# Kernel tuning notes

Measured on AMD Instinct MI355X. Metric: run time of the kernel, lower is better.

The kernel has to match this reference:

```python
import jax, jax.numpy as jnp
import numpy as np


def setup_inputs() -> dict:
    key = jax.random.key(0)
    ks = jax.random.split(key, 5)
    B, T, D, H = 64, 1024, 512, 1024
    s = 1.0 / np.sqrt(H)
    return {
        "x": jax.random.normal(ks[0], (B, T, D), dtype=jnp.float32),
        "W_ih": jax.random.normal(ks[1], (3 * H, D), dtype=jnp.float32) * s,
        "W_hh": jax.random.normal(ks[2], (3 * H, H), dtype=jnp.float32) * s,
        "b_ih": jax.random.normal(ks[3], (3 * H,), dtype=jnp.float32) * s,
        "b_hh": jax.random.normal(ks[4], (3 * H,), dtype=jnp.float32) * s,
    }


def reference(x, W_ih, W_hh, b_ih, b_hh):
    # GRULayer: per-timestep GRU cell recurrence, zero initial hidden state.
    B, T, D = x.shape
    H = W_hh.shape[1]
    h0 = jnp.zeros((B, H), dtype=x.dtype)
    xT = jnp.swapaxes(x, 0, 1)  # [T, B, D]

    def step(h, x_t):
        gi = x_t @ W_ih.T + b_ih          # [B, 3H]
        gh = h @ W_hh.T + b_hh            # [B, 3H]
        i_r, i_z, i_n = jnp.split(gi, 3, axis=-1)
        h_r, h_z, h_n = jnp.split(gh, 3, axis=-1)
        r = jax.nn.sigmoid(i_r + h_r)
        z = jax.nn.sigmoid(i_z + h_z)
        n = jnp.tanh(i_n + r * h_n)
        h_new = (1.0 - z) * n + z * h
        return h_new, h_new

    h_final, outs = jax.lax.scan(step, h0, xT)  # outs: [T, B, H]
    res = jnp.swapaxes(outs, 0, 1)              # [B, T, H]
    return res, h_final
```

## Files before the change

kernel.cpp:

```cpp
#include <hip/hip_runtime.h>
#include <hip/hip_bf16.h>

#define NB 64
#define TT 1024
#define ND 512
#define NH 1024
#define GRID 256
#define NTH 256

typedef float f32x4 __attribute__((ext_vector_type(4)));
typedef __bf16 bf16x8 __attribute__((ext_vector_type(8)));

__device__ __forceinline__ float sigmoid_f(float v) { return 1.0f / (1.0f + __expf(-v)); }

__device__ __forceinline__ float tanh_f(float v) {
    float a = fabsf(v);
    float e = __expf(-2.0f * a);
    float t = (1.0f - e) / (1.0f + e);
    return copysignf(t, v);
}

__device__ __forceinline__ f32x4 load_dwordx4_sc1(const void* p) {
    f32x4 r;
    asm volatile("global_load_dwordx4 %0, %1, off sc1" : "=v"(r) : "v"(p));
    return r;
}
__device__ __forceinline__ void store_short_sc1(void* p, unsigned v16) {
    asm volatile("global_store_short %0, %1, off sc1" :: "v"(p), "v"(v16) : "memory");
}
__device__ __forceinline__ void store_dword_sc1(unsigned* p, unsigned v) {
    asm volatile("global_store_dword %0, %1, off sc1" :: "v"(p), "v"(v) : "memory");
}
__device__ __forceinline__ unsigned load_dword_sc1_wait(const unsigned* p) {
    unsigned v;
    asm volatile("global_load_dword %0, %1, off sc1\n\ts_waitcnt vmcnt(0)"
                 : "=v"(v) : "v"(p) : "memory");
    return v;
}

__global__ void __launch_bounds__(NTH) gru_kernel(
    const float* __restrict__ x, const float* __restrict__ W_ih,
    const float* __restrict__ W_hh, const float* __restrict__ b_ih,
    const float* __restrict__ b_hh, float* __restrict__ out,
    unsigned* __restrict__ tags, __bf16* __restrict__ hbuf)
{
    extern __shared__ char smem[];
    __bf16* WihF = (__bf16*)smem;
    __bf16* WhhF = WihF + 4 * 4 * 3 * 64 * 8;
    float* prz = (float*)(WhhF + 4 * 8 * 3 * 64 * 8);
    float* pnx = prz + 2048;
    float* pnh = pnx + 1024;

    const int tid = threadIdx.x;
    const int bg = blockIdx.x >> 6;
    const int cg = blockIdx.x & 63;
    const int brow = bg << 4;
    const int hc0 = cg << 4;

    for (int s = tid; s < 4 * 4 * 3 * 64; s += NTH) {
        int ln = s & 63, r = s >> 6;
        int g = r % 3, r2 = r / 3;
        int it = r2 & 3, w = r2 >> 2;
        int k = w * 128 + it * 32 + (ln >> 4) * 8;
        int col = ln & 15;
        const float* src = W_ih + (size_t)(g * NH + hc0 + col) * ND + k;
        float4 va = *(const float4*)(src);
        float4 vb = *(const float4*)(src + 4);
        bf16x8 f;
        f[0] = (__bf16)va.x; f[1] = (__bf16)va.y; f[2] = (__bf16)va.z; f[3] = (__bf16)va.w;
        f[4] = (__bf16)vb.x; f[5] = (__bf16)vb.y; f[6] = (__bf16)vb.z; f[7] = (__bf16)vb.w;
        *(bf16x8*)(WihF + (size_t)s * 8) = f;
    }
    for (int s = tid; s < 4 * 8 * 3 * 64; s += NTH) {
        int ln = s & 63, r = s >> 6;
        int g = r % 3, r2 = r / 3;
        int it = r2 & 7, w = r2 >> 3;
        int k = w * 256 + it * 32 + (ln >> 4) * 8;
        int col = ln & 15;
        const float* src = W_hh + (size_t)(g * NH + hc0 + col) * NH + k;
        float4 va = *(const float4*)(src);
        float4 vb = *(const float4*)(src + 4);
        bf16x8 f;
        f[0] = (__bf16)va.x; f[1] = (__bf16)va.y; f[2] = (__bf16)va.z; f[3] = (__bf16)va.w;
        f[4] = (__bf16)vb.x; f[5] = (__bf16)vb.y; f[6] = (__bf16)vb.z; f[7] = (__bf16)vb.w;
        *(bf16x8*)(WhhF + (size_t)s * 8) = f;
    }

    const int jcol = tid & 15;
    const int mrow = tid >> 4;
    const float b_r = b_ih[hc0 + jcol] + b_hh[hc0 + jcol];
    const float b_z = b_ih[NH + hc0 + jcol] + b_hh[NH + hc0 + jcol];
    const float b_nx = b_ih[2 * NH + hc0 + jcol];
    const float b_nh = b_hh[2 * NH + hc0 + jcol];

    __syncthreads();

    const int wave = tid >> 6;
    const int lane = tid & 63;
    const int lrow = lane & 15;
    const int kgrp = lane >> 4;

    unsigned* mytag = tags + ((size_t)(bg * 64 + cg) * 16 + wave);
    const unsigned* polltag = tags + ((size_t)(bg * 64 + wave * 16 + (lane >> 2)) * 16 + (lane & 3));

    __bf16* hst0 = hbuf + (size_t)NB * NH + (size_t)(brow + mrow) * NH + hc0 + jcol;
    __bf16* hst1 = hbuf + (size_t)(brow + mrow) * NH + hc0 + jcol;

    float hp = 0.0f;

    f32x4 xa[4], xb[4];
    {
        const float* xr = x + ((size_t)(brow + lrow) * TT + 0) * ND + wave * 128 + kgrp * 8;
        #pragma unroll
        for (int it = 0; it < 4; ++it) {
            xa[it] = *(const f32x4*)(xr + it * 32);
            xb[it] = *(const f32x4*)(xr + it * 32 + 4);
        }
    }

    for (int t = 0; t < TT; ++t) {
        const int par = t & 1;
        f32x4 ar{}, az{}, anx{}, anh{};

        #pragma unroll
        for (int it = 0; it < 4; ++it) {
            bf16x8 af;
            af[0] = (__bf16)xa[it][0]; af[1] = (__bf16)xa[it][1];
            af[2] = (__bf16)xa[it][2]; af[3] = (__bf16)xa[it][3];
            af[4] = (__bf16)xb[it][0]; af[5] = (__bf16)xb[it][1];
            af[6] = (__bf16)xb[it][2]; af[7] = (__bf16)xb[it][3];
            const __bf16* wp = WihF + ((size_t)(wave * 4 + it) * 3) * 512 + lane * 8;
            bf16x8 wr = *(const bf16x8*)(wp);
            bf16x8 wz = *(const bf16x8*)(wp + 512);
            bf16x8 wn = *(const bf16x8*)(wp + 1024);
            ar  = __builtin_amdgcn_mfma_f32_16x16x32_bf16(af, wr, ar, 0, 0, 0);
            az  = __builtin_amdgcn_mfma_f32_16x16x32_bf16(af, wz, az, 0, 0, 0);
            anx = __builtin_amdgcn_mfma_f32_16x16x32_bf16(af, wn, anx, 0, 0, 0);
        }

        if (t > 0) {
            const unsigned tgt = (unsigned)t;
            for (;;) {
                unsigned v = load_dword_sc1_wait(polltag);
                if (__all(v == tgt)) break;
                __builtin_amdgcn_s_sleep(1);
            }
        }

        const __bf16* hrow = hbuf + (size_t)par * NB * NH + (size_t)(brow + lrow) * NH
                           + wave * 256 + kgrp * 8;
        f32x4 hraw[8];
        #pragma unroll
        for (int it = 0; it < 8; ++it)
            hraw[it] = load_dwordx4_sc1(hrow + it * 32);
        asm volatile("s_waitcnt vmcnt(0)" ::: "memory");
        __builtin_amdgcn_sched_barrier(0);
        #pragma unroll
        for (int it = 0; it < 8; ++it) {
            bf16x8 af = __builtin_bit_cast(bf16x8, hraw[it]);
            const __bf16* wp = WhhF + ((size_t)(wave * 8 + it) * 3) * 512 + lane * 8;
            bf16x8 wr = *(const bf16x8*)(wp);
            bf16x8 wz = *(const bf16x8*)(wp + 512);
            bf16x8 wn = *(const bf16x8*)(wp + 1024);
            ar  = __builtin_amdgcn_mfma_f32_16x16x32_bf16(af, wr, ar, 0, 0, 0);
            az  = __builtin_amdgcn_mfma_f32_16x16x32_bf16(af, wz, az, 0, 0, 0);
            anh = __builtin_amdgcn_mfma_f32_16x16x32_bf16(af, wn, anh, 0, 0, 0);
        }

        if (t + 1 < TT) {
            const float* xn = x + ((size_t)(brow + lrow) * TT + (t + 1)) * ND
                            + wave * 128 + kgrp * 8;
            #pragma unroll
            for (int it = 0; it < 4; ++it) {
                xa[it] = *(const f32x4*)(xn + it * 32);
                xb[it] = *(const f32x4*)(xn + it * 32 + 4);
            }
        }

        #pragma unroll
        for (int j = 0; j < 4; ++j) {
            int row = kgrp * 4 + j;
            prz[wave * 512 + row * 32 + lrow]      = ar[j];
            prz[wave * 512 + row * 32 + 16 + lrow] = az[j];
            pnx[wave * 256 + row * 16 + lrow]      = anx[j];
            pnh[wave * 256 + row * 16 + lrow]      = anh[j];
        }
        __syncthreads();

        {
            float rpre = prz[mrow * 32 + jcol] + prz[512 + mrow * 32 + jcol]
                       + prz[1024 + mrow * 32 + jcol] + prz[1536 + mrow * 32 + jcol] + b_r;
            float zpre = prz[mrow * 32 + 16 + jcol] + prz[512 + mrow * 32 + 16 + jcol]
                       + prz[1024 + mrow * 32 + 16 + jcol] + prz[1536 + mrow * 32 + 16 + jcol] + b_z;
            float ginn = pnx[mrow * 16 + jcol] + pnx[256 + mrow * 16 + jcol]
                       + pnx[512 + mrow * 16 + jcol] + pnx[768 + mrow * 16 + jcol] + b_nx;
            float ghnn = pnh[mrow * 16 + jcol] + pnh[256 + mrow * 16 + jcol]
                       + pnh[512 + mrow * 16 + jcol] + pnh[768 + mrow * 16 + jcol] + b_nh;
            float r = sigmoid_f(rpre);
            float z = sigmoid_f(zpre);
            float n = tanh_f(ginn + r * ghnn);
            float hn = (1.0f - z) * n + z * hp;
            hp = hn;

            unsigned hb = (unsigned)__builtin_bit_cast(unsigned short, (__bf16)hn);
            store_short_sc1(par ? hst1 : hst0, hb);
            asm volatile("s_waitcnt vmcnt(0)" ::: "memory");
            if (t < TT - 1 && lane == 0)
                store_dword_sc1(mytag, (unsigned)(t + 1));

            out[((size_t)(brow + mrow) * TT + t) * NH + hc0 + jcol] = hn;
            if (t == TT - 1)
                out[(size_t)NB * TT * NH + (size_t)(brow + mrow) * NH + hc0 + jcol] = hn;
        }

        __syncthreads();
    }
}

extern "C" void kernel_launch(void* const* d_in, const int* in_sizes, int n_in,
                              void* d_out, int out_size, void* d_ws, size_t ws_size,
                              hipStream_t stream) {
    (void)in_sizes; (void)n_in; (void)out_size;
    const float* x    = (const float*)d_in[0];
    const float* W_ih = (const float*)d_in[1];
    const float* W_hh = (const float*)d_in[2];
    const float* b_ih = (const float*)d_in[3];
    const float* b_hh = (const float*)d_in[4];
    float* out = (float*)d_out;

    unsigned* tags = (unsigned*)d_ws;
    __bf16* hbuf = (__bf16*)((char*)d_ws + 16384);
    const size_t clear_bytes = 16384 + (size_t)NB * NH * sizeof(__bf16);
    if (ws_size < 16384 + (size_t)2 * NB * NH * sizeof(__bf16)) return;
    hipMemsetAsync(d_ws, 0, clear_bytes, stream);

    const size_t smem_bytes = 163840;
    (void)hipFuncSetAttribute((const void*)gru_kernel,
                              hipFuncAttributeMaxDynamicSharedMemorySize, (int)smem_bytes);
    gru_kernel<<<GRID, NTH, smem_bytes, stream>>>(x, W_ih, W_hh, b_ih, b_hh, out, tags, hbuf);
}
```

Baseline: 3.751 ms.

## Embed step tags into hidden-state words to remove separate flag handshake

Each hidden value is now stored as a 32-bit word that carries the bf16 value in the low half and the timestep tag in the high half. Consumers read the data directly and check every tag, so the separate tag store, the wait on store completion, and the flag polling are gone. Readers fall back to polling a single word when the tags do not match. The next-step x prefetch is also moved before the wait. The cost is twice the hidden-buffer traffic and extra repacking ALU work, and correctness now depends on each 32-bit store being seen atomically.

```diff
diff --git a/kernel.cpp b/kernel.cpp
--- a/kernel.cpp
+++ b/kernel.cpp
@@ -9,6 +9,7 @@
 #define NTH 256
 
 typedef float f32x4 __attribute__((ext_vector_type(4)));
+typedef unsigned u32x4 __attribute__((ext_vector_type(4)));
 typedef __bf16 bf16x8 __attribute__((ext_vector_type(8)));
 
 __device__ __forceinline__ float sigmoid_f(float v) { return 1.0f / (1.0f + __expf(-v)); }
@@ -20,13 +21,11 @@
     return copysignf(t, v);
 }
 
-__device__ __forceinline__ f32x4 load_dwordx4_sc1(const void* p) {
-    f32x4 r;
-    asm volatile("global_load_dwordx4 %0, %1, off sc1" : "=v"(r) : "v"(p));
+__device__ __forceinline__ u32x4 load_dwordx4_sc1_off(const unsigned* p, int imm) {
+    u32x4 r;
+    asm volatile("global_load_dwordx4 %0, %1, off offset:%2 sc1"
+                 : "=v"(r) : "v"(p), "i"(imm));
     return r;
-}
-__device__ __forceinline__ void store_short_sc1(void* p, unsigned v16) {
-    asm volatile("global_store_short %0, %1, off sc1" :: "v"(p), "v"(v16) : "memory");
 }
 __device__ __forceinline__ void store_dword_sc1(unsigned* p, unsigned v) {
     asm volatile("global_store_dword %0, %1, off sc1" :: "v"(p), "v"(v) : "memory");
@@ -42,7 +41,7 @@
     const float* __restrict__ x, const float* __restrict__ W_ih,
     const float* __restrict__ W_hh, const float* __restrict__ b_ih,
     const float* __restrict__ b_hh, float* __restrict__ out,
-    unsigned* __restrict__ tags, __bf16* __restrict__ hbuf)
+    unsigned* __restrict__ hbuf)
 {
     extern __shared__ char smem[];
     __bf16* WihF = (__bf16*)smem;
@@ -100,11 +99,9 @@
     const int lrow = lane & 15;
     const int kgrp = lane >> 4;
 
-    unsigned* mytag = tags + ((size_t)(bg * 64 + cg) * 16 + wave);
-    const unsigned* polltag = tags + ((size_t)(bg * 64 + wave * 16 + (lane >> 2)) * 16 + (lane & 3));
-
-    __bf16* hst0 = hbuf + (size_t)NB * NH + (size_t)(brow + mrow) * NH + hc0 + jcol;
-    __bf16* hst1 = hbuf + (size_t)(brow + mrow) * NH + hc0 + jcol;
+    const size_t hoff_c = (size_t)(brow + lrow) * NH + wave * 256 + kgrp * 8;
+    const size_t hoff_cn = (size_t)(brow + 4 * (lane & 3)) * NH + wave * 256 + (lane >> 2) * 16;
+    const size_t hoff_p = (size_t)(brow + mrow) * NH + hc0 + jcol;
 
     float hp = 0.0f;
 
@@ -138,26 +135,57 @@
             anx = __builtin_amdgcn_mfma_f32_16x16x32_bf16(af, wn, anx, 0, 0, 0);
         }
 
-        if (t > 0) {
-            const unsigned tgt = (unsigned)t;
+        if (t + 1 < TT) {
+            const float* xn = x + ((size_t)(brow + lrow) * TT + (t + 1)) * ND
+                            + wave * 128 + kgrp * 8;
+            #pragma unroll
+            for (int it = 0; it < 4; ++it) {
+                xa[it] = *(const f32x4*)(xn + it * 32);
+                xb[it] = *(const f32x4*)(xn + it * 32 + 4);
+            }
+        }
+
+        const unsigned tag = (unsigned)t;
+        const unsigned* hbase = hbuf + (size_t)par * NB * NH + hoff_c;
+        const unsigned* cbase = hbuf + (size_t)par * NB * NH + hoff_cn;
+        u32x4 hw[16];
+        for (;;) {
+            hw[0]  = load_dwordx4_sc1_off(hbase,   0); hw[1]  = load_dwordx4_sc1_off(hbase,  16);
+            hw[2]  = load_dwordx4_sc1_off(hbase, 128); hw[3]  = load_dwordx4_sc1_off(hbase, 144);
+            hw[4]  = load_dwordx4_sc1_off(hbase, 256); hw[5]  = load_dwordx4_sc1_off(hbase, 272);
+            hw[6]  = load_dwordx4_sc1_off(hbase, 384); hw[7]  = load_dwordx4_sc1_off(hbase, 400);
+            hw[8]  = load_dwordx4_sc1_off(hbase, 512); hw[9]  = load_dwordx4_sc1_off(hbase, 528);
+            hw[10] = load_dwordx4_sc1_off(hbase, 640); hw[11] = load_dwordx4_sc1_off(hbase, 656);
+            hw[12] = load_dwordx4_sc1_off(hbase, 768); hw[13] = load_dwordx4_sc1_off(hbase, 784);
+            hw[14] = load_dwordx4_sc1_off(hbase, 896); hw[15] = load_dwordx4_sc1_off(hbase, 912);
+            asm volatile("s_waitcnt vmcnt(0)" ::: "memory");
+            __builtin_amdgcn_sched_barrier(0);
+            unsigned acc = 0;
+            #pragma unroll
+            for (int i = 0; i < 16; ++i) {
+                acc |= ((hw[i][0] >> 16) ^ tag);
+                acc |= ((hw[i][1] >> 16) ^ tag);
+                acc |= ((hw[i][2] >> 16) ^ tag);
+                acc |= ((hw[i][3] >> 16) ^ tag);
+            }
+            if (__all(acc == 0)) break;
             for (;;) {
-                unsigned v = load_dword_sc1_wait(polltag);
-                if (__all(v == tgt)) break;
+                unsigned c = load_dword_sc1_wait(cbase);
+                if (__all((c >> 16) == tag)) break;
                 __builtin_amdgcn_s_sleep(1);
             }
         }
-
-        const __bf16* hrow = hbuf + (size_t)par * NB * NH + (size_t)(brow + lrow) * NH
-                           + wave * 256 + kgrp * 8;
-        f32x4 hraw[8];
-        #pragma unroll
-        for (int it = 0; it < 8; ++it)
-            hraw[it] = load_dwordx4_sc1(hrow + it * 32);
-        asm volatile("s_waitcnt vmcnt(0)" ::: "memory");
         __builtin_amdgcn_sched_barrier(0);
+
         #pragma unroll
         for (int it = 0; it < 8; ++it) {
-            bf16x8 af = __builtin_bit_cast(bf16x8, hraw[it]);
+            u32x4 a = hw[2 * it], b = hw[2 * it + 1];
+            u32x4 d;
+            d[0] = (a[0] & 0xffffu) | (a[1] << 16);
+            d[1] = (a[2] & 0xffffu) | (a[3] << 16);
+            d[2] = (b[0] & 0xffffu) | (b[1] << 16);
+            d[3] = (b[2] & 0xffffu) | (b[3] << 16);
+            bf16x8 af = __builtin_bit_cast(bf16x8, d);
             const __bf16* wp = WhhF + ((size_t)(wave * 8 + it) * 3) * 512 + lane * 8;
             bf16x8 wr = *(const bf16x8*)(wp);
             bf16x8 wz = *(const bf16x8*)(wp + 512);
@@ -165,16 +193,6 @@
             ar  = __builtin_amdgcn_mfma_f32_16x16x32_bf16(af, wr, ar, 0, 0, 0);
             az  = __builtin_amdgcn_mfma_f32_16x16x32_bf16(af, wz, az, 0, 0, 0);
             anh = __builtin_amdgcn_mfma_f32_16x16x32_bf16(af, wn, anh, 0, 0, 0);
-        }
-
-        if (t + 1 < TT) {
-            const float* xn = x + ((size_t)(brow + lrow) * TT + (t + 1)) * ND
-                            + wave * 128 + kgrp * 8;
-            #pragma unroll
-            for (int it = 0; it < 4; ++it) {
-                xa[it] = *(const f32x4*)(xn + it * 32);
-                xb[it] = *(const f32x4*)(xn + it * 32 + 4);
-            }
         }
 
         #pragma unroll
@@ -202,12 +220,11 @@
             float hn = (1.0f - z) * n + z * hp;
             hp = hn;
 
-            unsigned hb = (unsigned)__builtin_bit_cast(unsigned short, (__bf16)hn);
-            store_short_sc1(par ? hst1 : hst0, hb);
-            asm volatile("s_waitcnt vmcnt(0)" ::: "memory");
-            if (t < TT - 1 && lane == 0)
-                store_dword_sc1(mytag, (unsigned)(t + 1));
-
+            if (t < TT - 1) {
+                unsigned hb = (unsigned)__builtin_bit_cast(unsigned short, (__bf16)hn);
+                unsigned hword = ((unsigned)(t + 1) << 16) | hb;
+                store_dword_sc1(hbuf + (size_t)((t + 1) & 1) * NB * NH + hoff_p, hword);
+            }
             out[((size_t)(brow + mrow) * TT + t) * NH + hc0 + jcol] = hn;
             if (t == TT - 1)
                 out[(size_t)NB * TT * NH + (size_t)(brow + mrow) * NH + hc0 + jcol] = hn;
@@ -228,14 +245,13 @@
     const float* b_hh = (const float*)d_in[4];
     float* out = (float*)d_out;
 
-    unsigned* tags = (unsigned*)d_ws;
-    __bf16* hbuf = (__bf16*)((char*)d_ws + 16384);
-    const size_t clear_bytes = 16384 + (size_t)NB * NH * sizeof(__bf16);
-    if (ws_size < 16384 + (size_t)2 * NB * NH * sizeof(__bf16)) return;
-    hipMemsetAsync(d_ws, 0, clear_bytes, stream);
+    unsigned* hbuf = (unsigned*)d_ws;
+    const size_t need = (size_t)2 * NB * NH * sizeof(unsigned);
+    if (ws_size < need) return;
+    hipMemsetAsync(d_ws, 0, need, stream);
 
     const size_t smem_bytes = 163840;
     (void)hipFuncSetAttribute((const void*)gru_kernel,
                               hipFuncAttributeMaxDynamicSharedMemorySize, (int)smem_bytes);
-    gru_kernel<<<GRID, NTH, smem_bytes, stream>>>(x, W_ih, W_hh, b_ih, b_hh, out, tags, hbuf);
-}
+    gru_kernel<<<GRID, NTH, smem_bytes, stream>>>(x, W_ih, W_hh, b_ih, b_hh, out, hbuf);
+}
```

New measurement: 5.261 ms. 1.4x slower.

## Replace tag-based inter-block sync with sentinel-valued triple-buffered hidden state

Applied to the files above, without the earlier changes.

Removes the separate per-wave tag flags. Consumers now detect readiness from the hidden-state data itself, using a sentinel value (0xFFFFFFFF) in a three-slot rotating buffer, and producers reset the slot two steps ahead back to the sentinel. Hidden-state writes are packed into dword stores via a lane shuffle, and the full wait-before-tag-store is replaced by a partial vmcnt wait. The aim is to cut one round trip (store data, wait, store tag, poll tag, load data) off the serial recurrence critical path. The risk is subtle memory-ordering issues, since the 32-bit sentinel check relies on dword-atomic visibility and on the two-step reset ordering.

```diff
diff --git a/kernel.cpp b/kernel.cpp
--- a/kernel.cpp
+++ b/kernel.cpp
@@ -7,8 +7,11 @@
 #define NH 1024
 #define GRID 256
 #define NTH 256
+#define HSLOT ((size_t)NB * NH * 2)
+#define SENT 0xFFFFFFFFu
 
 typedef float f32x4 __attribute__((ext_vector_type(4)));
+typedef unsigned u32x4 __attribute__((ext_vector_type(4)));
 typedef __bf16 bf16x8 __attribute__((ext_vector_type(8)));
 
 __device__ __forceinline__ float sigmoid_f(float v) { return 1.0f / (1.0f + __expf(-v)); }
@@ -20,18 +23,16 @@
     return copysignf(t, v);
 }
 
-__device__ __forceinline__ f32x4 load_dwordx4_sc1(const void* p) {
-    f32x4 r;
-    asm volatile("global_load_dwordx4 %0, %1, off sc1" : "=v"(r) : "v"(p));
+__device__ __forceinline__ u32x4 load_dwordx4_sc1_off(const void* p, int imm) {
+    u32x4 r;
+    asm volatile("global_load_dwordx4 %0, %1, off offset:%2 sc1"
+                 : "=v"(r) : "v"(p), "i"(imm));
     return r;
 }
-__device__ __forceinline__ void store_short_sc1(void* p, unsigned v16) {
-    asm volatile("global_store_short %0, %1, off sc1" :: "v"(p), "v"(v16) : "memory");
-}
-__device__ __forceinline__ void store_dword_sc1(unsigned* p, unsigned v) {
+__device__ __forceinline__ void store_dword_sc1(void* p, unsigned v) {
     asm volatile("global_store_dword %0, %1, off sc1" :: "v"(p), "v"(v) : "memory");
 }
-__device__ __forceinline__ unsigned load_dword_sc1_wait(const unsigned* p) {
+__device__ __forceinline__ unsigned load_dword_sc1_wait(const void* p) {
     unsigned v;
     asm volatile("global_load_dword %0, %1, off sc1\n\ts_waitcnt vmcnt(0)"
                  : "=v"(v) : "v"(p) : "memory");
@@ -42,7 +43,7 @@
     const float* __restrict__ x, const float* __restrict__ W_ih,
     const float* __restrict__ W_hh, const float* __restrict__ b_ih,
     const float* __restrict__ b_hh, float* __restrict__ out,
-    unsigned* __restrict__ tags, __bf16* __restrict__ hbuf)
+    unsigned char* __restrict__ hbase)
 {
     extern __shared__ char smem[];
     __bf16* WihF = (__bf16*)smem;
@@ -100,11 +101,10 @@
     const int lrow = lane & 15;
     const int kgrp = lane >> 4;
 
-    unsigned* mytag = tags + ((size_t)(bg * 64 + cg) * 16 + wave);
-    const unsigned* polltag = tags + ((size_t)(bg * 64 + wave * 16 + (lane >> 2)) * 16 + (lane & 3));
-
-    __bf16* hst0 = hbuf + (size_t)NB * NH + (size_t)(brow + mrow) * NH + hc0 + jcol;
-    __bf16* hst1 = hbuf + (size_t)(brow + mrow) * NH + hc0 + jcol;
+    const size_t coff = ((size_t)(brow + lrow) * NH + wave * 256 + kgrp * 8) * 2;
+    const size_t cnoff = ((size_t)(brow + 4 * (lane & 3)) * NH
+                        + ((size_t)wave * 16 + (lane >> 2)) * 16) * 2;
+    const size_t poff = ((size_t)(brow + mrow) * NH + hc0 + jcol) * 2;
 
     float hp = 0.0f;
 
@@ -119,7 +119,6 @@
     }
 
     for (int t = 0; t < TT; ++t) {
-        const int par = t & 1;
         f32x4 ar{}, az{}, anx{}, anh{};
 
         #pragma unroll
@@ -138,26 +137,38 @@
             anx = __builtin_amdgcn_mfma_f32_16x16x32_bf16(af, wn, anx, 0, 0, 0);
         }
 
-        if (t > 0) {
-            const unsigned tgt = (unsigned)t;
+        const unsigned char* hb_r = hbase + (size_t)(t % 3) * HSLOT + coff;
+        const unsigned char* cn_r = hbase + (size_t)(t % 3) * HSLOT + cnoff;
+        u32x4 hw[8];
+        for (;;) {
+            hw[0] = load_dwordx4_sc1_off(hb_r,   0);
+            hw[1] = load_dwordx4_sc1_off(hb_r,  64);
+            hw[2] = load_dwordx4_sc1_off(hb_r, 128);
+            hw[3] = load_dwordx4_sc1_off(hb_r, 192);
+            hw[4] = load_dwordx4_sc1_off(hb_r, 256);
+            hw[5] = load_dwordx4_sc1_off(hb_r, 320);
+            hw[6] = load_dwordx4_sc1_off(hb_r, 384);
+            hw[7] = load_dwordx4_sc1_off(hb_r, 448);
+            asm volatile("s_waitcnt vmcnt(0)" ::: "memory");
+            __builtin_amdgcn_sched_barrier(0);
+            unsigned bad = 0;
+            #pragma unroll
+            for (int i = 0; i < 8; ++i) {
+                bad |= (hw[i][0] == SENT) | (hw[i][1] == SENT)
+                     | (hw[i][2] == SENT) | (hw[i][3] == SENT);
+            }
+            if (__all(bad == 0)) break;
             for (;;) {
-                unsigned v = load_dword_sc1_wait(polltag);
-                if (__all(v == tgt)) break;
+                unsigned c = load_dword_sc1_wait(cn_r);
+                if (__all(c != SENT)) break;
                 __builtin_amdgcn_s_sleep(1);
             }
         }
-
-        const __bf16* hrow = hbuf + (size_t)par * NB * NH + (size_t)(brow + lrow) * NH
-                           + wave * 256 + kgrp * 8;
-        f32x4 hraw[8];
-        #pragma unroll
-        for (int it = 0; it < 8; ++it)
-            hraw[it] = load_dwordx4_sc1(hrow + it * 32);
-        asm volatile("s_waitcnt vmcnt(0)" ::: "memory");
         __builtin_amdgcn_sched_barrier(0);
+
         #pragma unroll
         for (int it = 0; it < 8; ++it) {
-            bf16x8 af = __builtin_bit_cast(bf16x8, hraw[it]);
+            bf16x8 af = __builtin_bit_cast(bf16x8, hw[it]);
             const __bf16* wp = WhhF + ((size_t)(wave * 8 + it) * 3) * 512 + lane * 8;
             bf16x8 wr = *(const bf16x8*)(wp);
             bf16x8 wz = *(const bf16x8*)(wp + 512);
@@ -167,6 +178,18 @@
             anh = __builtin_amdgcn_mfma_f32_16x16x32_bf16(af, wn, anh, 0, 0, 0);
         }
 
+        #pragma unroll
+        for (int j = 0; j < 4; ++j) {
+            int row = kgrp * 4 + j;
+            prz[wave * 512 + row * 32 + lrow]      = ar[j];
+            prz[wave * 512 + row * 32 + 16 + lrow] = az[j];
+            pnx[wave * 256 + row * 16 + lrow]      = anx[j];
+            pnh[wave * 256 + row * 16 + lrow]      = anh[j];
+        }
+        __syncthreads();
+
+        if (t <= TT - 3 && (jcol & 1) == 0)
+            store_dword_sc1(hbase + (size_t)((t + 2) % 3) * HSLOT + poff, SENT);
         if (t + 1 < TT) {
             const float* xn = x + ((size_t)(brow + lrow) * TT + (t + 1)) * ND
                             + wave * 128 + kgrp * 8;
@@ -176,16 +199,6 @@
                 xb[it] = *(const f32x4*)(xn + it * 32 + 4);
             }
         }
-
-        #pragma unroll
-        for (int j = 0; j < 4; ++j) {
-            int row = kgrp * 4 + j;
-            prz[wave * 512 + row * 32 + lrow]      = ar[j];
-            prz[wave * 512 + row * 32 + 16 + lrow] = az[j];
-            pnx[wave * 256 + row * 16 + lrow]      = anx[j];
-            pnh[wave * 256 + row * 16 + lrow]      = anh[j];
-        }
-        __syncthreads();
 
         {
             float rpre = prz[mrow * 32 + jcol] + prz[512 + mrow * 32 + jcol]
@@ -202,12 +215,14 @@
             float hn = (1.0f - z) * n + z * hp;
             hp = hn;
 
-            unsigned hb = (unsigned)__builtin_bit_cast(unsigned short, (__bf16)hn);
-            store_short_sc1(par ? hst1 : hst0, hb);
-            asm volatile("s_waitcnt vmcnt(0)" ::: "memory");
-            if (t < TT - 1 && lane == 0)
-                store_dword_sc1(mytag, (unsigned)(t + 1));
-
+            unsigned hb16 = (unsigned)__builtin_bit_cast(unsigned short, (__bf16)hn);
+            unsigned nb16 = (unsigned)__shfl_xor((int)hb16, 1);
+            if (t < TT - 1) {
+                asm volatile("s_waitcnt vmcnt(8)" ::: "memory");
+                if ((jcol & 1) == 0)
+                    store_dword_sc1(hbase + (size_t)((t + 1) % 3) * HSLOT + poff,
+                                    hb16 | (nb16 << 16));
+            }
             out[((size_t)(brow + mrow) * TT + t) * NH + hc0 + jcol] = hn;
             if (t == TT - 1)
                 out[(size_t)NB * TT * NH + (size_t)(brow + mrow) * NH + hc0 + jcol] = hn;
@@ -228,14 +243,13 @@
     const float* b_hh = (const float*)d_in[4];
     float* out = (float*)d_out;
 
-    unsigned* tags = (unsigned*)d_ws;
-    __bf16* hbuf = (__bf16*)((char*)d_ws + 16384);
-    const size_t clear_bytes = 16384 + (size_t)NB * NH * sizeof(__bf16);
-    if (ws_size < 16384 + (size_t)2 * NB * NH * sizeof(__bf16)) return;
-    hipMemsetAsync(d_ws, 0, clear_bytes, stream);
+    unsigned char* hbase = (unsigned char*)d_ws;
+    if (ws_size < 3 * HSLOT) return;
+    hipMemsetAsync(hbase, 0x00, HSLOT, stream);
+    hipMemsetAsync(hbase + HSLOT, 0xFF, 2 * HSLOT, stream);
 
     const size_t smem_bytes = 163840;
     (void)hipFuncSetAttribute((const void*)gru_kernel,
                               hipFuncAttributeMaxDynamicSharedMemorySize, (int)smem_bytes);
-    gru_kernel<<<GRID, NTH, smem_bytes, stream>>>(x, W_ih, W_hh, b_ih, b_hh, out, tags, hbuf);
-}
+    gru_kernel<<<GRID, NTH, smem_bytes, stream>>>(x, W_ih, W_hh, b_ih, b_hh, out, hbase);
+}
```

After: 3.884 ms. +3.5%, slower.
